# Optimization experiments

Measured on AMD Instinct MI355X. Metric: run time of the kernel, lower is better.

## Reference

```python
import jax, jax.numpy as jnp
import numpy as np

D_MODEL, D_STATE, D_CONV, EXPAND = 1024, 16, 4, 2
D_INNER = EXPAND * D_MODEL  # 2048
DT_RANK = (D_MODEL + 15) // 16  # 64
B_SZ, L = 2, 4096


def setup_inputs() -> dict:
    key = jax.random.key(0)
    ks = jax.random.split(key, 10)
    x = jax.random.normal(ks[0], (B_SZ, L, D_MODEL), dtype=jnp.float32)
    in_proj_w = jax.random.normal(ks[1], (2 * D_INNER, D_MODEL), dtype=jnp.float32) * 0.02
    conv_w = jax.random.normal(ks[2], (D_INNER, D_CONV), dtype=jnp.float32) * 0.2
    conv_b = jax.random.normal(ks[3], (D_INNER,), dtype=jnp.float32) * 0.02
    x_proj_w = jax.random.normal(ks[4], (DT_RANK + 2 * D_STATE, D_INNER), dtype=jnp.float32) * 0.02
    dt_std = DT_RANK ** -0.5
    dt_proj_w = jax.random.uniform(ks[5], (D_INNER, DT_RANK), minval=-dt_std, maxval=dt_std, dtype=jnp.float32)
    # dt bias init: inverse softplus of dt sampled log-uniform in [1e-3, 1e-1]
    dt = jnp.exp(jax.random.uniform(ks[6], (D_INNER,)) * (np.log(0.1) - np.log(0.001)) + np.log(0.001))
    dt = jnp.clip(dt, 1e-4, None)
    dt_proj_b = dt + jnp.log(-jnp.expm1(-dt))
    A_log = jnp.log(jnp.broadcast_to(jnp.arange(1, D_STATE + 1, dtype=jnp.float32), (D_INNER, D_STATE)))
    Dp = jnp.ones((D_INNER,), dtype=jnp.float32)
    out_proj_w = jax.random.normal(ks[7], (D_MODEL, D_INNER), dtype=jnp.float32) * 0.02
    return {"x": x, "in_proj_w": in_proj_w, "conv_w": conv_w, "conv_b": conv_b,
            "x_proj_w": x_proj_w, "dt_proj_w": dt_proj_w, "dt_proj_b": dt_proj_b,
            "A_log": A_log, "Dp": Dp, "out_proj_w": out_proj_w}


def _mamba(x, in_proj_w, conv_w, conv_b, x_proj_w, dt_proj_w, dt_proj_b, A_log, Dp, out_proj_w):
    b, l, _ = x.shape
    xz = jnp.einsum('bld,ed->ble', x, in_proj_w)          # (b, l, 2*d_inner)
    u, z = jnp.split(xz, 2, axis=-1)                       # each (b, l, d_inner)
    # causal depthwise conv along l
    uc = jnp.transpose(u, (0, 2, 1))                       # (b, d, l)
    kern = conv_w[:, None, :]                              # (d, 1, w)
    uc = jax.lax.conv_general_dilated(
        uc, kern, window_strides=(1,), padding=[(D_CONV - 1, 0)],
        dimension_numbers=('NCH', 'OIH', 'NCH'), feature_group_count=D_INNER)
    uc = uc + conv_b[None, :, None]
    u_act = jax.nn.silu(jnp.transpose(uc, (0, 2, 1)))      # (b, l, d_inner)
    # projections for dt, B, C
    x_dbl = jnp.einsum('bld,ed->ble', u_act, x_proj_w)     # (b, l, dt_rank + 2n)
    dt_lo = x_dbl[..., :DT_RANK]
    Bm = x_dbl[..., DT_RANK:DT_RANK + D_STATE]             # (b, l, n)
    Cm = x_dbl[..., DT_RANK + D_STATE:]                    # (b, l, n)
    dt = jnp.einsum('blr,dr->bld', dt_lo, dt_proj_w)       # (b, l, d_inner)
    delta = jax.nn.softplus(dt + dt_proj_b)                # (b, l, d_inner)
    A = -jnp.exp(A_log)                                    # (d_inner, n)

    def step(h, inp):
        d_t, B_t, C_t, u_t = inp                           # (b,d), (b,n), (b,n), (b,d)
        dA = jnp.exp(d_t[..., None] * A)                   # (b, d, n)
        h = h * dA + (d_t * u_t)[..., None] * B_t[:, None, :]
        y = jnp.einsum('bdn,bn->bd', h, C_t)
        return h, y

    xs = (jnp.transpose(delta, (1, 0, 2)), jnp.transpose(Bm, (1, 0, 2)),
          jnp.transpose(Cm, (1, 0, 2)), jnp.transpose(u_act, (1, 0, 2)))
    h0 = jnp.zeros((b, D_INNER, D_STATE), dtype=x.dtype)
    _, ys = jax.lax.scan(step, h0, xs)                     # (l, b, d)
    y = jnp.transpose(ys, (1, 0, 2)) + u_act * Dp          # (b, l, d_inner)
    y = y * jax.nn.silu(z)
    return jnp.einsum('bld,ed->ble', y, out_proj_w)        # (b, l, d_model)


def reference(x, in_proj_w, conv_w, conv_b, x_proj_w, dt_proj_w, dt_proj_b, A_log, Dp, out_proj_w):
    return _mamba(x, in_proj_w, conv_w, conv_b, x_proj_w, dt_proj_w, dt_proj_b, A_log, Dp, out_proj_w)
```

## Files before the change

### kernel.cpp

```cpp
#include <hip/hip_runtime.h>

#define D_MODEL  1024
#define D_STATE  16
#define D_CONV   4
#define D_INNER  2048
#define DT_RANK  64
#define B_SZ     2
#define L_SEQ    4096
#define NPROJ    96
#define M_ROWS   (B_SZ * L_SEQ)
#define NC       64
#define LC       64

typedef __bf16 bf16;
typedef __bf16 bf16x8 __attribute__((ext_vector_type(8)));
typedef __bf16 bf16x4 __attribute__((ext_vector_type(4)));
typedef __bf16 bf16x2 __attribute__((ext_vector_type(2)));
typedef float  f32x4  __attribute__((ext_vector_type(4)));
typedef float  f32x2  __attribute__((ext_vector_type(2)));

__device__ __forceinline__ void gload16(const void* g, void* l) {
    __builtin_amdgcn_global_load_lds(
        (const __attribute__((address_space(1))) unsigned int*)g,
        (__attribute__((address_space(3))) unsigned int*)l,
        16, 0, 0);
}

__global__ __launch_bounds__(256)
void f2b_all(const float4* __restrict__ s0, bf16x4* __restrict__ d0, int n0,
             const float4* __restrict__ s1, bf16x4* __restrict__ d1, int n1,
             const float4* __restrict__ s2, bf16x4* __restrict__ d2, int n2,
             const float4* __restrict__ s3, bf16x4* __restrict__ d3, int n3) {
    int j = blockIdx.x * 256 + threadIdx.x;
    const float4* s; bf16x4* d;
    if (j < n0) { s = s0; d = d0; }
    else {
        j -= n0;
        if (j < n1) { s = s1; d = d1; }
        else {
            j -= n1;
            if (j < n2) { s = s2; d = d2; }
            else {
                j -= n2;
                if (j >= n3) return;
                s = s3; d = d3;
            }
        }
    }
    float4 v = s[j];
    bf16x4 o = {(bf16)v.x, (bf16)v.y, (bf16)v.z, (bf16)v.w};
    d[j] = o;
}

__global__ __launch_bounds__(256) void f2b_pad_xproj(const float* __restrict__ in,
                                                     bf16* __restrict__ out) {
    int i = blockIdx.x * 256 + threadIdx.x;
    int row = i >> 11, col = i & 2047;
    float v = (row < NPROJ) ? in[row * 2048 + col] : 0.f;
    out[i] = (bf16)v;
}

template <int MODE, int WM>
__global__ __launch_bounds__(WM * 128, 2)
void gemm_bt(const bf16* __restrict__ A, const bf16* __restrict__ B,
             int M, int N, int K, int lda, int ldb,
             float* __restrict__ outf, bf16* __restrict__ outb,
             const float* __restrict__ bias, int ldout) {
    constexpr int NW      = WM * 2;
    constexpr int A_TILES = WM * 4;
    constexpr int B_TILES = 8;
    constexpr int UPW     = (A_TILES + B_TILES) * 2 / NW;

    __shared__ bf16 As[A_TILES * 2 * 64 * 8];
    __shared__ bf16 Bs[B_TILES * 2 * 64 * 8];

    const int tid  = threadIdx.x;
    const int wave = tid >> 6;
    const int lane = tid & 63;
    const int l15  = lane & 15;
    const int lk   = lane >> 4;
    const int mBase = blockIdx.y * (WM * 64);
    const int nBase = blockIdx.x * 128;
    const int koff  = blockIdx.z * K;
    const int wm    = wave >> 1;
    const int wn    = wave & 1;

    f32x4 acc[4][4];
    const f32x4 zz = {0.f, 0.f, 0.f, 0.f};
#pragma unroll
    for (int i = 0; i < 4; i++)
#pragma unroll
        for (int j = 0; j < 4; j++) acc[i][j] = zz;

    for (int k0 = 0; k0 < K; k0 += 64) {
#pragma unroll
        for (int u = 0; u < UPW; u++) {
            const int g = wave * UPW + u;
            const int s = g & 1;
            const int t = g >> 1;
            if (t < A_TILES) {
                const bf16* gA = A + (size_t)(mBase + t * 16 + l15) * lda
                                   + koff + k0 + s * 32 + lk * 8;
                gload16(gA, &As[((t * 2 + s) * 64 + lane) * 8]);
            } else {
                const int nt = t - A_TILES;
                const bf16* gB = B + (size_t)(nBase + nt * 16 + l15) * ldb
                                   + koff + k0 + s * 32 + lk * 8;
                gload16(gB, &Bs[((nt * 2 + s) * 64 + lane) * 8]);
            }
        }
        __syncthreads();

#pragma unroll
        for (int s = 0; s < 2; s++) {
            bf16x8 af[4], bfr[4];
#pragma unroll
            for (int i = 0; i < 4; i++)
                af[i] = *(const bf16x8*)&As[(((wm * 4 + i) * 2 + s) * 64 + lane) * 8];
#pragma unroll
            for (int j = 0; j < 4; j++)
                bfr[j] = *(const bf16x8*)&Bs[(((wn * 4 + j) * 2 + s) * 64 + lane) * 8];
#pragma unroll
            for (int i = 0; i < 4; i++)
#pragma unroll
                for (int j = 0; j < 4; j++)
                    acc[i][j] = __builtin_amdgcn_mfma_f32_16x16x32_bf16(af[i], bfr[j],
                                                                        acc[i][j], 0, 0, 0);
        }
        __syncthreads();
    }

#pragma unroll
    for (int i = 0; i < 4; i++) {
#pragma unroll
        for (int j = 0; j < 4; j++) {
            const int col = nBase + wn * 64 + j * 16 + l15;
#pragma unroll
            for (int r = 0; r < 4; r++) {
                const int row = mBase + wm * 64 + i * 16 + lk * 4 + r;
                float v = acc[i][j][r];
                if (MODE == 0) {
                    outb[(size_t)row * ldout + col] = (bf16)v;
                } else if (MODE == 2) {
                    float xv = v + bias[col];
                    float sp = fmaxf(xv, 0.f) + log1pf(expf(-fabsf(xv)));
                    outb[(size_t)row * ldout + col] = (bf16)sp;
                } else if (MODE == 3) {
                    outf[(size_t)row * ldout + col] = v;
                } else {
                    outf[((size_t)blockIdx.z * M + row) * 128 + col] = v;
                }
            }
        }
    }
}

__global__ __launch_bounds__(256)
void reduce_xproj(const float* __restrict__ part, float* __restrict__ xdbl,
                  bf16* __restrict__ xdbl_b) {
    int i = blockIdx.x * 256 + threadIdx.x;
    if (i >= M_ROWS * NPROJ) return;
    int row = i / NPROJ;
    int col = i - row * NPROJ;
    size_t o = (size_t)row * 128 + col;
    float s = part[o] + part[(size_t)M_ROWS * 128 + o]
            + part[(size_t)2 * M_ROWS * 128 + o] + part[(size_t)3 * M_ROWS * 128 + o];
    xdbl[i] = s;
    xdbl_b[i] = (bf16)s;
}

__global__ __launch_bounds__(256)
void conv_silu(const bf16* __restrict__ xz, const float* __restrict__ cw,
               const float* __restrict__ cb, bf16* __restrict__ uact) {
    int i = blockIdx.x * 256 + threadIdx.x;
    int dp = i & 1023;
    int l  = (i >> 10) & (L_SEQ - 1);
    int b  = i >> 22;
    float4 w0 = *(const float4*)&cw[dp * 8];
    float4 w1 = *(const float4*)&cw[dp * 8 + 4];
    const float wv0[4] = {w0.x, w0.y, w0.z, w0.w};
    const float wv1[4] = {w1.x, w1.y, w1.z, w1.w};
    float2 cbv = *(const float2*)&cb[dp * 2];
    float a0 = cbv.x, a1 = cbv.y;
    size_t rb = (size_t)b * L_SEQ;
    const unsigned int* xz32 = (const unsigned int*)xz;
#pragma unroll
    for (int k = 0; k < 4; k++) {
        int li = l - 3 + k;
        if (li >= 0) {
            unsigned int u = xz32[(rb + li) * 2048 + dp];
            float lo = __uint_as_float(u << 16);
            float hi = __uint_as_float(u & 0xFFFF0000u);
            a0 += lo * wv0[k];
            a1 += hi * wv1[k];
        }
    }
    float s0 = a0 / (1.f + expf(-a0));
    float s1 = a1 / (1.f + expf(-a1));
    bf16x2 pk = {(bf16)s0, (bf16)s1};
    ((bf16x2*)uact)[(rb + l) * 1024 + dp] = pk;
}

__global__ __launch_bounds__(256)
void scan_passA(const bf16* __restrict__ delta, const bf16* __restrict__ uact,
                const float* __restrict__ xdbl, const float* __restrict__ A_log,
                float* __restrict__ hloc, float* __restrict__ Ssum) {
    __shared__ float sB[LC][16];
    int tid = threadIdx.x, bid = blockIdx.x;
    int d = (bid & 7) * 256 + tid;
    int c = (bid >> 3) & (NC - 1);
    int b = bid >> 9;
    size_t rowb = (size_t)b * L_SEQ + c * LC;
    for (int i = tid; i < LC * 16; i += 256)
        sB[i >> 4][i & 15] = xdbl[(rowb + (i >> 4)) * NPROJ + DT_RANK + (i & 15)];
    float a[16];
    bool regular = true;
#pragma unroll
    for (int n = 0; n < 16; n++) {
        a[n] = expf(A_log[d * 16 + n]);
        regular = regular && (fabsf(a[n] - (float)(n + 1) * a[0]) < 1e-3f * (n + 1));
    }
    f32x2 h2[8];
#pragma unroll
    for (int k = 0; k < 8; k++) h2[k] = {0.f, 0.f};
    float S = 0.f;
    __syncthreads();

    if (regular) {
        const float na0 = -a[0] * 1.44269504f;
        for (int t = 0; t < LC; t++) {
            size_t r = rowb + t;
            float dt = (float)delta[r * D_INNER + d];
            float u  = (float)uact [r * D_INNER + d];
            S += dt;
            f32x2 du2 = {dt * u, dt * u};
            const f32x2* B2 = (const f32x2*)&sB[t][0];
            float e  = exp2f(dt * na0);
            float e2 = e * e;
            f32x2 p  = {e, e2};
            f32x2 ee = {e2, e2};
#pragma unroll
            for (int k = 0; k < 8; k++) {
                h2[k] = h2[k] * p + du2 * B2[k];
                p = p * ee;
            }
        }
    } else {
        f32x2 An2[8];
#pragma unroll
        for (int k = 0; k < 8; k++)
            An2[k] = {-a[2 * k] * 1.44269504f, -a[2 * k + 1] * 1.44269504f};
        for (int t = 0; t < LC; t++) {
            size_t r = rowb + t;
            float dt = (float)delta[r * D_INNER + d];
            float u  = (float)uact [r * D_INNER + d];
            S += dt;
            f32x2 du2 = {dt * u, dt * u};
            const f32x2* B2 = (const f32x2*)&sB[t][0];
#pragma unroll
            for (int k = 0; k < 8; k++) {
                f32x2 dA = {exp2f(dt * An2[k][0]), exp2f(dt * An2[k][1])};
                h2[k] = h2[k] * dA + du2 * B2[k];
            }
        }
    }
    size_t cb_ = (size_t)b * NC + c;
#pragma unroll
    for (int k = 0; k < 8; k++) {
        hloc[(cb_ * 16 + 2 * k    ) * D_INNER + d] = h2[k][0];
        hloc[(cb_ * 16 + 2 * k + 1) * D_INNER + d] = h2[k][1];
    }
    Ssum[cb_ * D_INNER + d] = S;
}

__global__ __launch_bounds__(256)
void scan_mid(const float* __restrict__ hloc, const float* __restrict__ Ssum,
              const float* __restrict__ A_log, float* __restrict__ h0) {
    int idx = blockIdx.x * 256 + threadIdx.x;
    int d = idx & (D_INNER - 1);
    int n = (idx >> 11) & 15;
    int b = idx >> 15;
    float An = -expf(A_log[d * 16 + n]) * 1.44269504f;
    float H = 0.f;
    for (int c = 0; c < NC; c++) {
        size_t cb_ = (size_t)b * NC + c;
        h0[(cb_ * 16 + n) * D_INNER + d] = H;
        H = H * exp2f(Ssum[cb_ * D_INNER + d] * An)
          + hloc[(cb_ * 16 + n) * D_INNER + d];
    }
}

__global__ __launch_bounds__(256)
void scan_passB(const bf16* __restrict__ delta, const bf16* __restrict__ uact,
                const float* __restrict__ xdbl, const float* __restrict__ A_log,
                const float* __restrict__ h0, const float* __restrict__ Dp,
                const bf16* __restrict__ xz, bf16* __restrict__ y) {
    __shared__ float sBC[LC][32];
    int tid = threadIdx.x, bid = blockIdx.x;
    int d = (bid & 7) * 256 + tid;
    int c = (bid >> 3) & (NC - 1);
    int b = bid >> 9;
    size_t rowb = (size_t)b * L_SEQ + c * LC;
    for (int i = tid; i < LC * 32; i += 256)
        sBC[i >> 5][i & 31] = xdbl[(rowb + (i >> 5)) * NPROJ + DT_RANK + (i & 31)];
    float a[16];
    bool regular = true;
#pragma unroll
    for (int n = 0; n < 16; n++) {
        a[n] = expf(A_log[d * 16 + n]);
        regular = regular && (fabsf(a[n] - (float)(n + 1) * a[0]) < 1e-3f * (n + 1));
    }
    size_t cb_ = (size_t)b * NC + c;
    f32x2 h2[8];
#pragma unroll
    for (int k = 0; k < 8; k++) {
        h2[k][0] = h0[(cb_ * 16 + 2 * k    ) * D_INNER + d];
        h2[k][1] = h0[(cb_ * 16 + 2 * k + 1) * D_INNER + d];
    }
    float Dd = Dp[d];
    __syncthreads();

    if (regular) {
        const float na0 = -a[0] * 1.44269504f;
        for (int t = 0; t < LC; t++) {
            size_t r = rowb + t;
            float dt = (float)delta[r * D_INNER + d];
            float u  = (float)uact [r * D_INNER + d];
            f32x2 du2 = {dt * u, dt * u};
            const f32x2* B2 = (const f32x2*)&sBC[t][0];
            const f32x2* C2 = (const f32x2*)&sBC[t][16];
            float e  = exp2f(dt * na0);
            float e2 = e * e;
            f32x2 p  = {e, e2};
            f32x2 ee = {e2, e2};
            f32x2 yt2 = {0.f, 0.f};
#pragma unroll
            for (int k = 0; k < 8; k++) {
                h2[k] = h2[k] * p + du2 * B2[k];
                yt2 = yt2 + h2[k] * C2[k];
                p = p * ee;
            }
            float yt = yt2[0] + yt2[1] + u * Dd;
            float z = (float)xz[r * (2 * D_INNER) + D_INNER + d];
            float g = z / (1.f + expf(-z));
            y[r * D_INNER + d] = (bf16)(yt * g);
        }
    } else {
        f32x2 An2[8];
#pragma unroll
        for (int k = 0; k < 8; k++)
            An2[k] = {-a[2 * k] * 1.44269504f, -a[2 * k + 1] * 1.44269504f};
        for (int t = 0; t < LC; t++) {
            size_t r = rowb + t;
            float dt = (float)delta[r * D_INNER + d];
            float u  = (float)uact [r * D_INNER + d];
            f32x2 du2 = {dt * u, dt * u};
            const f32x2* B2 = (const f32x2*)&sBC[t][0];
            const f32x2* C2 = (const f32x2*)&sBC[t][16];
            f32x2 yt2 = {0.f, 0.f};
#pragma unroll
            for (int k = 0; k < 8; k++) {
                f32x2 dA = {exp2f(dt * An2[k][0]), exp2f(dt * An2[k][1])};
                h2[k] = h2[k] * dA + du2 * B2[k];
                yt2 = yt2 + h2[k] * C2[k];
            }
            float yt = yt2[0] + yt2[1] + u * Dd;
            float z = (float)xz[r * (2 * D_INNER) + D_INNER + d];
            float g = z / (1.f + expf(-z));
            y[r * D_INNER + d] = (bf16)(yt * g);
        }
    }
}

extern "C" void kernel_launch(void* const* d_in, const int* in_sizes, int n_in,
                              void* d_out, int out_size, void* d_ws, size_t ws_size,
                              hipStream_t stream) {
    const float* x         = (const float*)d_in[0];
    const float* in_proj_w = (const float*)d_in[1];
    const float* conv_w    = (const float*)d_in[2];
    const float* conv_b    = (const float*)d_in[3];
    const float* x_proj_w  = (const float*)d_in[4];
    const float* dt_proj_w = (const float*)d_in[5];
    const float* dt_proj_b = (const float*)d_in[6];
    const float* A_log     = (const float*)d_in[7];
    const float* Dp        = (const float*)d_in[8];
    const float* out_proj_w= (const float*)d_in[9];
    float* out             = (float*)d_out;

    char* p = (char*)d_ws;
    auto alloc = [&](size_t bytes) -> char* {
        char* r = p;
        p += (bytes + 255) & ~(size_t)255;
        return r;
    };
    bf16*  x_bf    = (bf16*) alloc((size_t)M_ROWS * D_MODEL * 2);
    bf16*  w_in    = (bf16*) alloc((size_t)2 * D_INNER * D_MODEL * 2);
    bf16*  w_xp    = (bf16*) alloc((size_t)128 * D_INNER * 2);
    bf16*  w_dt    = (bf16*) alloc((size_t)D_INNER * DT_RANK * 2);
    bf16*  w_out   = (bf16*) alloc((size_t)D_MODEL * D_INNER * 2);
    bf16*  xz      = (bf16*) alloc((size_t)M_ROWS * 2 * D_INNER * 2);
    bf16*  uact    = (bf16*) alloc((size_t)M_ROWS * D_INNER * 2);
    float* xdbl    = (float*)alloc((size_t)M_ROWS * NPROJ * 4);
    bf16*  xdbl_b  = (bf16*) alloc((size_t)M_ROWS * NPROJ * 2);
    bf16*  deltab  = (bf16*) alloc((size_t)M_ROWS * D_INNER * 2);
    float* hloc    = (float*)alloc((size_t)B_SZ * NC * 16 * D_INNER * 4);
    float* Ssum    = (float*)alloc((size_t)B_SZ * NC * D_INNER * 4);
    float* h0      = (float*)alloc((size_t)B_SZ * NC * 16 * D_INNER * 4);
    bf16*  ybf     = (bf16*) alloc((size_t)M_ROWS * D_INNER * 2);
    float* partial = hloc;

    {
        const int n0 = M_ROWS * D_MODEL / 4;
        const int n1 = 2 * D_INNER * D_MODEL / 4;
        const int n2 = D_INNER * DT_RANK / 4;
        const int n3 = D_MODEL * D_INNER / 4;
        const int nt = n0 + n1 + n2 + n3;
        f2b_all<<<(nt + 255) / 256, 256, 0, stream>>>(
            (const float4*)x, (bf16x4*)x_bf, n0,
            (const float4*)in_proj_w, (bf16x4*)w_in, n1,
            (const float4*)dt_proj_w, (bf16x4*)w_dt, n2,
            (const float4*)out_proj_w, (bf16x4*)w_out, n3);
        f2b_pad_xproj<<<(128 * D_INNER) / 256, 256, 0, stream>>>(x_proj_w, w_xp);
    }

    gemm_bt<0, 4><<<dim3(2 * D_INNER / 128, M_ROWS / 256, 1), 512, 0, stream>>>(
        x_bf, w_in, M_ROWS, 2 * D_INNER, D_MODEL, D_MODEL, D_MODEL,
        nullptr, xz, nullptr, 2 * D_INNER);

    conv_silu<<<(M_ROWS * D_INNER / 2) / 256, 256, 0, stream>>>(xz, conv_w, conv_b, uact);

    gemm_bt<4, 2><<<dim3(1, M_ROWS / 128, 4), 256, 0, stream>>>(
        uact, w_xp, M_ROWS, 128, 512, D_INNER, D_INNER,
        partial, nullptr, nullptr, 128);
    reduce_xproj<<<(M_ROWS * NPROJ + 255) / 256, 256, 0, stream>>>(partial, xdbl, xdbl_b);

    gemm_bt<2, 4><<<dim3(D_INNER / 128, M_ROWS / 256, 1), 512, 0, stream>>>(
        xdbl_b, w_dt, M_ROWS, D_INNER, DT_RANK, NPROJ, DT_RANK,
        nullptr, deltab, dt_proj_b, D_INNER);

    scan_passA<<<B_SZ * NC * (D_INNER / 256), 256, 0, stream>>>(
        deltab, uact, xdbl, A_log, hloc, Ssum);
    scan_mid<<<(B_SZ * D_INNER * 16) / 256, 256, 0, stream>>>(hloc, Ssum, A_log, h0);
    scan_passB<<<B_SZ * NC * (D_INNER / 256), 256, 0, stream>>>(
        deltab, uact, xdbl, A_log, h0, Dp, xz, ybf);

    gemm_bt<3, 2><<<dim3(D_MODEL / 128, M_ROWS / 128, 1), 256, 0, stream>>>(
        ybf, w_out, M_ROWS, D_MODEL, D_INNER, D_INNER, D_INNER,
        out, nullptr, nullptr, D_MODEL);

    (void)in_sizes; (void)n_in; (void)out_size; (void)ws_size;
}
```

Before: 494.9 us.

## Use atomic split-K for x_proj and out_proj, halve scan chunk count

The x_proj split-K GEMM now accumulates directly into the zeroed xdbl buffer with float atomics instead of writing partials and running a separate reduction kernel. A small conversion kernel produces the bf16 copy. The output projection becomes a 2-way split-K with atomics into the zeroed output, to raise block count. The dt GEMM uses smaller 128-row tiles, and the scan uses 32 chunks of 128 steps instead of 64 of 64. Atomic accumulation makes summation order nondeterministic and adds memset cost. Fewer scan chunks cut mid-pass work but reduce scan parallelism.

```diff
diff --git a/kernel.cpp b/kernel.cpp
--- a/kernel.cpp
+++ b/kernel.cpp
@@ -9,8 +9,8 @@
 #define L_SEQ    4096
 #define NPROJ    96
 #define M_ROWS   (B_SZ * L_SEQ)
-#define NC       64
-#define LC       64
+#define NC       32
+#define LC       128
 
 typedef __bf16 bf16;
 typedef __bf16 bf16x8 __attribute__((ext_vector_type(8)));
@@ -60,12 +60,22 @@
     out[i] = (bf16)v;
 }
 
+__global__ __launch_bounds__(256)
+void xdbl_to_b(const float4* __restrict__ in, bf16x4* __restrict__ out, int n4) {
+    int i = blockIdx.x * 256 + threadIdx.x;
+    if (i < n4) {
+        float4 v = in[i];
+        bf16x4 o = {(bf16)v.x, (bf16)v.y, (bf16)v.z, (bf16)v.w};
+        out[i] = o;
+    }
+}
+
 template <int MODE, int WM>
 __global__ __launch_bounds__(WM * 128, 2)
 void gemm_bt(const bf16* __restrict__ A, const bf16* __restrict__ B,
              int M, int N, int K, int lda, int ldb,
              float* __restrict__ outf, bf16* __restrict__ outb,
-             const float* __restrict__ bias, int ldout) {
+             const float* __restrict__ bias, int ldout, int nvalid) {
     constexpr int NW      = WM * 2;
     constexpr int A_TILES = WM * 4;
     constexpr int B_TILES = 8;
@@ -148,25 +158,12 @@
                 } else if (MODE == 3) {
                     outf[(size_t)row * ldout + col] = v;
                 } else {
-                    outf[((size_t)blockIdx.z * M + row) * 128 + col] = v;
+                    if (col < nvalid)
+                        atomicAdd(&outf[(size_t)row * ldout + col], v);
                 }
             }
         }
     }
-}
-
-__global__ __launch_bounds__(256)
-void reduce_xproj(const float* __restrict__ part, float* __restrict__ xdbl,
-                  bf16* __restrict__ xdbl_b) {
-    int i = blockIdx.x * 256 + threadIdx.x;
-    if (i >= M_ROWS * NPROJ) return;
-    int row = i / NPROJ;
-    int col = i - row * NPROJ;
-    size_t o = (size_t)row * 128 + col;
-    float s = part[o] + part[(size_t)M_ROWS * 128 + o]
-            + part[(size_t)2 * M_ROWS * 128 + o] + part[(size_t)3 * M_ROWS * 128 + o];
-    xdbl[i] = s;
-    xdbl_b[i] = (bf16)s;
 }
 
 __global__ __launch_bounds__(256)
@@ -209,7 +206,7 @@
     int tid = threadIdx.x, bid = blockIdx.x;
     int d = (bid & 7) * 256 + tid;
     int c = (bid >> 3) & (NC - 1);
-    int b = bid >> 9;
+    int b = bid >> 8;
     size_t rowb = (size_t)b * L_SEQ + c * LC;
     for (int i = tid; i < LC * 16; i += 256)
         sB[i >> 4][i & 15] = xdbl[(rowb + (i >> 4)) * NPROJ + DT_RANK + (i & 15)];
@@ -299,7 +296,7 @@
     int tid = threadIdx.x, bid = blockIdx.x;
     int d = (bid & 7) * 256 + tid;
     int c = (bid >> 3) & (NC - 1);
-    int b = bid >> 9;
+    int b = bid >> 8;
     size_t rowb = (size_t)b * L_SEQ + c * LC;
     for (int i = tid; i < LC * 32; i += 256)
         sBC[i >> 5][i & 31] = xdbl[(rowb + (i >> 5)) * NPROJ + DT_RANK + (i & 31)];
@@ -407,7 +404,9 @@
     float* Ssum    = (float*)alloc((size_t)B_SZ * NC * D_INNER * 4);
     float* h0      = (float*)alloc((size_t)B_SZ * NC * 16 * D_INNER * 4);
     bf16*  ybf     = (bf16*) alloc((size_t)M_ROWS * D_INNER * 2);
-    float* partial = hloc;
+
+    hipMemsetAsync(xdbl, 0, (size_t)M_ROWS * NPROJ * 4, stream);
+    hipMemsetAsync(out, 0, (size_t)M_ROWS * D_MODEL * 4, stream);
 
     {
         const int n0 = M_ROWS * D_MODEL / 4;
@@ -425,18 +424,19 @@
 
     gemm_bt<0, 4><<<dim3(2 * D_INNER / 128, M_ROWS / 256, 1), 512, 0, stream>>>(
         x_bf, w_in, M_ROWS, 2 * D_INNER, D_MODEL, D_MODEL, D_MODEL,
-        nullptr, xz, nullptr, 2 * D_INNER);
+        nullptr, xz, nullptr, 2 * D_INNER, 2 * D_INNER);
 
     conv_silu<<<(M_ROWS * D_INNER / 2) / 256, 256, 0, stream>>>(xz, conv_w, conv_b, uact);
 
-    gemm_bt<4, 2><<<dim3(1, M_ROWS / 128, 4), 256, 0, stream>>>(
+    gemm_bt<5, 2><<<dim3(1, M_ROWS / 128, 4), 256, 0, stream>>>(
         uact, w_xp, M_ROWS, 128, 512, D_INNER, D_INNER,
-        partial, nullptr, nullptr, 128);
-    reduce_xproj<<<(M_ROWS * NPROJ + 255) / 256, 256, 0, stream>>>(partial, xdbl, xdbl_b);
-
-    gemm_bt<2, 4><<<dim3(D_INNER / 128, M_ROWS / 256, 1), 512, 0, stream>>>(
+        xdbl, nullptr, nullptr, NPROJ, NPROJ);
+    xdbl_to_b<<<(M_ROWS * NPROJ / 4 + 255) / 256, 256, 0, stream>>>(
+        (const float4*)xdbl, (bf16x4*)xdbl_b, M_ROWS * NPROJ / 4);
+
+    gemm_bt<2, 2><<<dim3(D_INNER / 128, M_ROWS / 128, 1), 256, 0, stream>>>(
         xdbl_b, w_dt, M_ROWS, D_INNER, DT_RANK, NPROJ, DT_RANK,
-        nullptr, deltab, dt_proj_b, D_INNER);
+        nullptr, deltab, dt_proj_b, D_INNER, D_INNER);
 
     scan_passA<<<B_SZ * NC * (D_INNER / 256), 256, 0, stream>>>(
         deltab, uact, xdbl, A_log, hloc, Ssum);
@@ -444,9 +444,9 @@
     scan_passB<<<B_SZ * NC * (D_INNER / 256), 256, 0, stream>>>(
         deltab, uact, xdbl, A_log, h0, Dp, xz, ybf);
 
-    gemm_bt<3, 2><<<dim3(D_MODEL / 128, M_ROWS / 128, 1), 256, 0, stream>>>(
-        ybf, w_out, M_ROWS, D_MODEL, D_INNER, D_INNER, D_INNER,
-        out, nullptr, nullptr, D_MODEL);
+    gemm_bt<5, 2><<<dim3(D_MODEL / 128, M_ROWS / 128, 2), 256, 0, stream>>>(
+        ybf, w_out, M_ROWS, D_MODEL, 1024, D_INNER, D_INNER,
+        out, nullptr, nullptr, D_MODEL, D_MODEL);
 
     (void)in_sizes; (void)n_in; (void)out_size; (void)ws_size;
 }
```

New measurement: 567.5 us. 1.15x slower.
